# Kernel tuning notes

Hardware: AMD Instinct MI355X
Metric: run time of the kernel (lower is better)

## Reference

```python
import jax, jax.numpy as jnp
import numpy as np

DIM = 1024
N_HEADS = 16
N_KV = 4
HEAD_DIM = DIM // N_HEADS          # 64
GROUP = N_HEADS // N_KV            # 4
KV_DIM = N_KV * HEAD_DIM           # 256
B, S = 2, 2048


def setup_inputs() -> dict:
    key = jax.random.key(0)
    ks = jax.random.split(key, 5)
    scale = 1.0 / np.sqrt(DIM)
    return {
        "x": jax.random.normal(ks[0], (B, S, DIM), dtype=jnp.float32),
        "W_qkv": jax.random.normal(ks[1], (DIM, DIM + 2 * KV_DIM), dtype=jnp.float32) * scale,
        "b_qkv": jnp.zeros((DIM + 2 * KV_DIM,), dtype=jnp.float32),
        "W_out": jax.random.normal(ks[2], (DIM, DIM), dtype=jnp.float32) * scale,
        "b_out": jnp.zeros((DIM,), dtype=jnp.float32),
    }


def reference(x, W_qkv, b_qkv, W_out, b_out):
    b, s, d = x.shape
    qkv = x @ W_qkv + b_qkv                                   # [b, s, dim + 2*kv_dim]
    q, k, v = jnp.split(qkv, [DIM, DIM + KV_DIM], axis=-1)
    # q: [b, n_kv, group, s, hd]; k, v: [b, n_kv, s, hd]
    q = q.reshape(b, s, N_HEADS, HEAD_DIM).transpose(0, 2, 1, 3)
    q = q.reshape(b, N_KV, GROUP, s, HEAD_DIM)
    k = k.reshape(b, s, N_KV, HEAD_DIM).transpose(0, 2, 1, 3)
    v = v.reshape(b, s, N_KV, HEAD_DIM).transpose(0, 2, 1, 3)
    scores = jnp.einsum("bkgsd,bktd->bkgst", q, k) / np.sqrt(HEAD_DIM)
    causal = jnp.tril(jnp.ones((s, s), dtype=bool))           # [s, s]
    scores = jnp.where(causal, scores, -jnp.inf)
    attn = jax.nn.softmax(scores, axis=-1)                    # dropout = 0 (eval)
    y = jnp.einsum("bkgst,bktd->bkgsd", attn, v)              # [b, n_kv, g, s, hd]
    y = y.reshape(b, N_HEADS, s, HEAD_DIM).transpose(0, 2, 1, 3).reshape(b, s, d)
    return y @ W_out + b_out
```

## Files before the change

### kernel.cpp

```cpp
#include <hip/hip_runtime.h>
#include <cstdint>
#include <cstddef>

typedef __bf16 bf16x8 __attribute__((ext_vector_type(8)));
typedef __bf16 bf16x4 __attribute__((ext_vector_type(4)));
typedef float  f32x4  __attribute__((ext_vector_type(4)));

#define DIMD 1024
#define SEQ  2048
#define NB   2
#define NH   16
#define HD   64
#define QKVN 1536
#define VOFF 1280
#define VSTR 2080
#define CSC  0.18033688011112042f

typedef __attribute__((address_space(1))) const void* as1_cvp;
typedef __attribute__((address_space(3))) void* as3_vp;
#define GLL16(g, l) __builtin_amdgcn_global_load_lds((as1_cvp)(const void*)(g), (as3_vp)(void*)(l), 16, 0, 0)

__global__ __launch_bounds__(256) void prep(
    const float* __restrict__ x, __bf16* __restrict__ xb,
    const float* __restrict__ Wqkv, __bf16* __restrict__ wqkvT,
    const float* __restrict__ Wout, __bf16* __restrict__ woutT)
{
    __shared__ float t[32][33];
    const int bidx = blockIdx.x;
    const int tid  = threadIdx.x;

    if (bidx < 4096) {
        int i = bidx * 256 + tid;
        float4 v = reinterpret_cast<const float4*>(x)[i];
        bf16x4 o;
        o[0] = (__bf16)v.x; o[1] = (__bf16)v.y; o[2] = (__bf16)v.z; o[3] = (__bf16)v.w;
        reinterpret_cast<bf16x4*>(xb)[i] = o;
        return;
    }

    const float* in; __bf16* out; int C, bx, by;
    if (bidx < 5632) {
        int idx = bidx - 4096;
        in = Wqkv; out = wqkvT; C = QKVN;
        bx = idx % 48; by = idx / 48;
    } else {
        int idx = bidx - 5632;
        in = Wout; out = woutT; C = DIMD;
        bx = idx & 31; by = idx >> 5;
    }
    const int tx = tid & 31, ty = tid >> 5;
#pragma unroll
    for (int i = 0; i < 32; i += 8)
        t[ty + i][tx] = in[(size_t)(by * 32 + ty + i) * C + bx * 32 + tx];
    __syncthreads();
#pragma unroll
    for (int i = 0; i < 32; i += 8)
        out[(size_t)(bx * 32 + ty + i) * DIMD + by * 32 + tx] = (__bf16)t[tx][ty + i];
}

__global__ void transpose_v(const __bf16* __restrict__ qkv, __bf16* __restrict__ vtg) {
    __shared__ __bf16 t[32][34];
    const int z = blockIdx.z;
    const int b = z >> 2, kh = z & 3;
    const int s0 = blockIdx.x * 32, d0 = blockIdx.y * 32;
    const int tx = threadIdx.x, ty = threadIdx.y;
    const __bf16* src = qkv + (size_t)b * SEQ * QKVN + VOFF + kh * HD;
#pragma unroll
    for (int i = 0; i < 32; i += 8)
        t[ty + i][tx] = src[(size_t)(s0 + ty + i) * QKVN + d0 + tx];
    __syncthreads();
    __bf16* dst = vtg + ((size_t)z * HD + d0) * VSTR + s0;
#pragma unroll
    for (int i = 0; i < 32; i += 8)
        dst[(size_t)(ty + i) * VSTR + tx] = t[tx][ty + i];
}

template<int OUT_BF16, int QSCALE>
__global__ __launch_bounds__(256) void gemm_bf16(
    const __bf16* __restrict__ A, const __bf16* __restrict__ Bt,
    const float* __restrict__ bias, void* __restrict__ Cout,
    int M, int N, int K, int nx)
{
    __shared__ __bf16 Als[128 * 32];
    __shared__ __bf16 Bls[64 * 32];
    const int tid  = threadIdx.x;
    const int lane = tid & 63;
    const int wave = tid >> 6;
    const int lo = lane & 15, hi = lane >> 4;

    const int lin = blockIdx.x;
    const int cpx = gridDim.x >> 3;
    const int swz = (lin & 7) * cpx + (lin >> 3);
    const int bm = (swz / nx) * 128, bn = (swz % nx) * 64;
    const int wr = (wave >> 1) * 64, wc = (wave & 1) * 32;

    const __bf16* gA = A  + (size_t)(bm + wave * 16 + (lane >> 2)) * K + (lane & 3) * 8;
    const __bf16* gB = Bt + (size_t)(bn + wave * 16 + (lane >> 2)) * K + (lane & 3) * 8;
    __bf16* lA = &Als[wave * 16 * 32];
    __bf16* lB = &Bls[wave * 16 * 32];

    f32x4 acc[4][2] = {};

    for (int k0 = 0; k0 < K; k0 += 32) {
        __syncthreads();
        GLL16(gA + k0,                  lA);
        GLL16(gA + k0 + (size_t)64 * K, lA + 2048);
        GLL16(gB + k0,                  lB);
        __syncthreads();

        bf16x8 af[4], bfr[2];
#pragma unroll
        for (int i = 0; i < 4; i++)
            af[i] = *reinterpret_cast<const bf16x8*>(&Als[(wr + i * 16 + lo) * 32 + hi * 8]);
#pragma unroll
        for (int j = 0; j < 2; j++)
            bfr[j] = *reinterpret_cast<const bf16x8*>(&Bls[(wc + j * 16 + lo) * 32 + hi * 8]);
#pragma unroll
        for (int i = 0; i < 4; i++)
#pragma unroll
            for (int j = 0; j < 2; j++)
                acc[i][j] = __builtin_amdgcn_mfma_f32_16x16x32_bf16(af[i], bfr[j], acc[i][j], 0, 0, 0);
    }

#pragma unroll
    for (int j = 0; j < 2; j++) {
        int col = bn + wc + j * 16 + lo;
        float bv = bias[col];
#pragma unroll
        for (int i = 0; i < 4; i++) {
            int row0 = bm + wr + i * 16 + hi * 4;
#pragma unroll
            for (int rr = 0; rr < 4; rr++) {
                float v = acc[i][j][rr] + bv;
                if (QSCALE && col < DIMD) v *= CSC;
                if (OUT_BF16) ((__bf16*)Cout)[(size_t)(row0 + rr) * N + col] = (__bf16)v;
                else          ((float* )Cout)[(size_t)(row0 + rr) * N + col] = v;
            }
        }
    }
}

__global__ __launch_bounds__(512, 4) void attn_fwd(
    const __bf16* __restrict__ qkv, const __bf16* __restrict__ vt, __bf16* __restrict__ y)
{
    __shared__ __bf16 Kls[128 * 64];
    __shared__ __bf16 Vls[64 * 128];
    __shared__ __bf16 Pls[8][2][16][72];
    const int tid  = threadIdx.x;
    const int wave = tid >> 6, lane = tid & 63;
    const int lo = lane & 15, hi = lane >> 4;
    const int head = wave & 3, par = wave >> 2;

    const int bid = blockIdx.x;
    const int z  = bid & 7;
    const int b  = z >> 2, kh = z & 3;
    const int p  = bid >> 3;
    const int h  = kh * 4 + head;

    const int TA = p, TB = 127 - p;
    const int qwA = TA * 16, qwB = TB * 16;
    const int cA = (TA >> 2) + 1, cB = (TB >> 2) + 1;
    const int nsc = (cB + 1) >> 1;

    const __bf16* base = qkv + (size_t)b * SEQ * QKVN;
    const __bf16* qp = base + h * HD;
    const __bf16* kp = base + DIMD + kh * HD;
    const __bf16* vp = vt + (size_t)z * HD * VSTR;

    const int srow = lane >> 3;
    const int sun  = ((lane & 7) ^ srow) * 8;
    const __bf16* kst0 = kp + (size_t)(wave * 16 + srow) * QKVN + sun;
    const __bf16* kst1 = kp + (size_t)(wave * 16 + 8 + srow) * QKVN + sun;
    const int vrow = lane >> 4;
    const int vun0 = ((lane & 15) ^ vrow) * 8;
    const int vun1 = ((lane & 15) ^ (vrow + 4)) * 8;
    const __bf16* vst0 = vp + (size_t)(wave * 8 + vrow) * VSTR + vun0;
    const __bf16* vst1 = vp + (size_t)(wave * 8 + 4 + vrow) * VSTR + vun1;
    __bf16* kdst = &Kls[wave * 1024];
    __bf16* vdst = &Vls[wave * 1024];

#define STAGE(s)                                            \
    do {                                                    \
        const size_t ko = (size_t)(s) * 128 * QKVN;         \
        const int    vo = (s) * 128;                        \
        GLL16(kst0 + ko, kdst);                             \
        GLL16(kst1 + ko, kdst + 512);                       \
        GLL16(vst0 + vo, vdst);                             \
        GLL16(vst1 + vo, vdst + 512);                       \
    } while (0)

    const int xk = lo & 7;
    const int u0 = (hi ^ xk) * 8;
    const int u1 = ((hi + 4) ^ xk) * 8;
    const int kb = par * 64;

    bf16x8 bQA0 = *reinterpret_cast<const bf16x8*>(qp + (size_t)(qwA + lo) * QKVN + hi * 8);
    bf16x8 bQA1 = *reinterpret_cast<const bf16x8*>(qp + (size_t)(qwA + lo) * QKVN + 32 + hi * 8);
    bf16x8 bQB0 = *reinterpret_cast<const bf16x8*>(qp + (size_t)(qwB + lo) * QKVN + hi * 8);
    bf16x8 bQB1 = *reinterpret_cast<const bf16x8*>(qp + (size_t)(qwB + lo) * QKVN + 32 + hi * 8);

    f32x4 accA[4] = {}, accB[4] = {};
    float ssA = 0.0f, ssB = 0.0f;

    STAGE(0);
    __syncthreads();

    for (int s = 0; s < nsc; ++s) {
        const int ce = 2 * s + par;
        const int kt = ce << 6;
        const bool aB = (ce < cB), dB = (ce == cB - 1);
        const bool aA = (ce < cA), dA = (ce == cA - 1);

        if (aB) {
#pragma unroll
            for (int ks = 0; ks < 4; ks++) {
                const __bf16* Kr = &Kls[(kb + ks * 16 + lo) * 64];
                bf16x8 aK0 = *reinterpret_cast<const bf16x8*>(Kr + u0);
                bf16x8 aK1 = *reinterpret_cast<const bf16x8*>(Kr + u1);

                {
                    f32x4 sv = {0.f, 0.f, 0.f, 0.f};
                    sv = __builtin_amdgcn_mfma_f32_16x16x32_bf16(aK0, bQB0, sv, 0, 0, 0);
                    sv = __builtin_amdgcn_mfma_f32_16x16x32_bf16(aK1, bQB1, sv, 0, 0, 0);
                    bf16x4 pk;
#pragma unroll
                    for (int r = 0; r < 4; r++) {
                        float e = exp2f(sv[r]);
                        if (dB && (kt + ks * 16 + hi * 4 + r > qwB + lo)) e = 0.0f;
                        ssB += e;
                        pk[r] = (__bf16)e;
                    }
                    *reinterpret_cast<bf16x4*>(&Pls[wave][1][lo][ks * 16 + hi * 4]) = pk;
                }
                if (aA) {
                    f32x4 sv = {0.f, 0.f, 0.f, 0.f};
                    sv = __builtin_amdgcn_mfma_f32_16x16x32_bf16(aK0, bQA0, sv, 0, 0, 0);
                    sv = __builtin_amdgcn_mfma_f32_16x16x32_bf16(aK1, bQA1, sv, 0, 0, 0);
                    bf16x4 pk;
#pragma unroll
                    for (int r = 0; r < 4; r++) {
                        float e = exp2f(sv[r]);
                        if (dA && (kt + ks * 16 + hi * 4 + r > qwA + lo)) e = 0.0f;
                        ssA += e;
                        pk[r] = (__bf16)e;
                    }
                    *reinterpret_cast<bf16x4*>(&Pls[wave][0][lo][ks * 16 + hi * 4]) = pk;
                }
            }

#pragma unroll
            for (int k2 = 0; k2 < 2; k2++) {
                const int uv = ((8 * par + k2 * 4 + hi) ^ xk) * 8;
                bf16x8 v0 = *reinterpret_cast<const bf16x8*>(&Vls[(0 * 16 + lo) * 128] + uv);
                bf16x8 v1 = *reinterpret_cast<const bf16x8*>(&Vls[(1 * 16 + lo) * 128] + uv);
                bf16x8 v2 = *reinterpret_cast<const bf16x8*>(&Vls[(2 * 16 + lo) * 128] + uv);
                bf16x8 v3 = *reinterpret_cast<const bf16x8*>(&Vls[(3 * 16 + lo) * 128] + uv);
                bf16x8 pB = *reinterpret_cast<const bf16x8*>(&Pls[wave][1][lo][k2 * 32 + hi * 8]);
                accB[0] = __builtin_amdgcn_mfma_f32_16x16x32_bf16(pB, v0, accB[0], 0, 0, 0);
                accB[1] = __builtin_amdgcn_mfma_f32_16x16x32_bf16(pB, v1, accB[1], 0, 0, 0);
                accB[2] = __builtin_amdgcn_mfma_f32_16x16x32_bf16(pB, v2, accB[2], 0, 0, 0);
                accB[3] = __builtin_amdgcn_mfma_f32_16x16x32_bf16(pB, v3, accB[3], 0, 0, 0);
                if (aA) {
                    bf16x8 pA = *reinterpret_cast<const bf16x8*>(&Pls[wave][0][lo][k2 * 32 + hi * 8]);
                    accA[0] = __builtin_amdgcn_mfma_f32_16x16x32_bf16(pA, v0, accA[0], 0, 0, 0);
                    accA[1] = __builtin_amdgcn_mfma_f32_16x16x32_bf16(pA, v1, accA[1], 0, 0, 0);
                    accA[2] = __builtin_amdgcn_mfma_f32_16x16x32_bf16(pA, v2, accA[2], 0, 0, 0);
                    accA[3] = __builtin_amdgcn_mfma_f32_16x16x32_bf16(pA, v3, accA[3], 0, 0, 0);
                }
            }
        }

        __syncthreads();
        if (s + 1 < nsc) {
            STAGE(s + 1);
            __syncthreads();
        }
    }
#undef STAGE

    float* cls = (float*)&Pls[0][0][0][0];
    const int cbase = (head * 64 + lane) * 36;
    if (par == 1) {
#pragma unroll
        for (int f = 0; f < 4; f++) {
            *reinterpret_cast<f32x4*>(&cls[cbase + f * 4])      = accA[f];
            *reinterpret_cast<f32x4*>(&cls[cbase + 16 + f * 4]) = accB[f];
        }
        cls[cbase + 32] = ssA;
        cls[cbase + 33] = ssB;
    }
    __syncthreads();
    if (par == 0) {
#pragma unroll
        for (int f = 0; f < 4; f++) {
            accA[f] += *reinterpret_cast<f32x4*>(&cls[cbase + f * 4]);
            accB[f] += *reinterpret_cast<f32x4*>(&cls[cbase + 16 + f * 4]);
        }
        ssA += cls[cbase + 32];
        ssB += cls[cbase + 33];

        ssA += __shfl_xor(ssA, 16);  ssA += __shfl_xor(ssA, 32);
        ssB += __shfl_xor(ssB, 16);  ssB += __shfl_xor(ssB, 32);
#pragma unroll
        for (int r = 0; r < 4; r++) {
            float srA = __shfl(ssA, hi * 4 + r);
            float srB = __shfl(ssB, hi * 4 + r);
            float invA = 1.0f / srA, invB = 1.0f / srB;
            int qA = qwA + hi * 4 + r, qB = qwB + hi * 4 + r;
#pragma unroll
            for (int f = 0; f < 4; f++) {
                y[(size_t)(b * SEQ + qA) * DIMD + h * HD + f * 16 + lo] = (__bf16)(accA[f][r] * invA);
                y[(size_t)(b * SEQ + qB) * DIMD + h * HD + f * 16 + lo] = (__bf16)(accB[f][r] * invB);
            }
        }
    }
}

extern "C" void kernel_launch(void* const* d_in, const int* in_sizes, int n_in,
                              void* d_out, int out_size, void* d_ws, size_t ws_size,
                              hipStream_t stream) {
    const float* x    = (const float*)d_in[0];
    const float* Wqkv = (const float*)d_in[1];
    const float* bqkv = (const float*)d_in[2];
    const float* Wout = (const float*)d_in[3];
    const float* bout = (const float*)d_in[4];
    float* out = (float*)d_out;

    char* ws = (char*)d_ws;
    __bf16* xb    = (__bf16*)(ws);
    __bf16* wqkvT = (__bf16*)(ws + ((size_t)8  << 20));
    __bf16* woutT = (__bf16*)(ws + ((size_t)11 << 20));
    __bf16* qkvb  = (__bf16*)(ws + ((size_t)13 << 20));
    __bf16* vtg   = wqkvT;
    __bf16* yb    = xb;

    const int M = NB * SEQ;

    prep<<<6656, 256, 0, stream>>>(x, xb, Wqkv, wqkvT, Wout, woutT);

    gemm_bf16<1, 1><<<(M / 128) * (QKVN / 64), 256, 0, stream>>>(
        xb, wqkvT, bqkv, qkvb, M, QKVN, DIMD, QKVN / 64);

    transpose_v<<<dim3(SEQ / 32, HD / 32, NB * 4), dim3(32, 8), 0, stream>>>(qkvb, vtg);

    attn_fwd<<<512, 512, 0, stream>>>(qkvb, vtg, yb);

    gemm_bf16<0, 0><<<(M / 128) * (DIMD / 64), 256, 0, stream>>>(
        yb, woutT, bout, out, M, DIMD, DIMD, DIMD / 64);
}
```

Before: 104.0 us.

## Double-buffer K/V tiles and keep P in registers via transposed PV MFMA

Doubles the K/V shared-memory buffers so the next tile's async global-to-LDS loads are issued before computing on the current tile, removing one barrier per iteration. The P-through-LDS round trip is dropped by computing O^T with 16x16x16 MFMAs that take the exp'd scores directly from registers as the B operand, with V as the A operand. Output stores become vectorized bf16x4 writes along the transposed layout. This trades wider MFMAs for more, smaller ones, raises LDS use, and needs a correct swizzled V fragment indexing.

```diff
diff --git a/kernel.cpp b/kernel.cpp
--- a/kernel.cpp
+++ b/kernel.cpp
@@ -5,6 +5,7 @@
 typedef __bf16 bf16x8 __attribute__((ext_vector_type(8)));
 typedef __bf16 bf16x4 __attribute__((ext_vector_type(4)));
 typedef float  f32x4  __attribute__((ext_vector_type(4)));
+typedef short  s16x4  __attribute__((ext_vector_type(4)));
 
 #define DIMD 1024
 #define SEQ  2048
@@ -143,9 +144,8 @@
 __global__ __launch_bounds__(512, 4) void attn_fwd(
     const __bf16* __restrict__ qkv, const __bf16* __restrict__ vt, __bf16* __restrict__ y)
 {
-    __shared__ __bf16 Kls[128 * 64];
-    __shared__ __bf16 Vls[64 * 128];
-    __shared__ __bf16 Pls[8][2][16][72];
+    __shared__ __bf16 Ka[2][8192];
+    __shared__ __bf16 Va[2][8192];
     const int tid  = threadIdx.x;
     const int wave = tid >> 6, lane = tid & 63;
     const int lo = lane & 15, hi = lane >> 4;
@@ -176,23 +176,26 @@
     const int vun1 = ((lane & 15) ^ (vrow + 4)) * 8;
     const __bf16* vst0 = vp + (size_t)(wave * 8 + vrow) * VSTR + vun0;
     const __bf16* vst1 = vp + (size_t)(wave * 8 + 4 + vrow) * VSTR + vun1;
-    __bf16* kdst = &Kls[wave * 1024];
-    __bf16* vdst = &Vls[wave * 1024];
-
-#define STAGE(s)                                            \
-    do {                                                    \
-        const size_t ko = (size_t)(s) * 128 * QKVN;         \
-        const int    vo = (s) * 128;                        \
-        GLL16(kst0 + ko, kdst);                             \
-        GLL16(kst1 + ko, kdst + 512);                       \
-        GLL16(vst0 + vo, vdst);                             \
-        GLL16(vst1 + vo, vdst + 512);                       \
+    __bf16* kdst = &Ka[0][wave * 1024];
+    __bf16* vdst = &Va[0][wave * 1024];
+
+#define STAGE(s, buf)                                              \
+    do {                                                           \
+        const size_t ko = (size_t)(s) * 128 * QKVN;                \
+        const int    vo = (s) * 128;                               \
+        GLL16(kst0 + ko, kdst + (buf) * 8192);                     \
+        GLL16(kst1 + ko, kdst + (buf) * 8192 + 512);               \
+        GLL16(vst0 + vo, vdst + (buf) * 8192);                     \
+        GLL16(vst1 + vo, vdst + (buf) * 8192 + 512);               \
     } while (0)
 
     const int xk = lo & 7;
     const int u0 = (hi ^ xk) * 8;
     const int u1 = ((hi + 4) ^ xk) * 8;
-    const int kb = par * 64;
+    int voff[4];
+#pragma unroll
+    for (int ks = 0; ks < 4; ks++)
+        voff[ks] = (((par * 8 + ks * 2 + (hi >> 1)) ^ xk) << 3) + (hi & 1) * 4;
 
     bf16x8 bQA0 = *reinterpret_cast<const bf16x8*>(qp + (size_t)(qwA + lo) * QKVN + hi * 8);
     bf16x8 bQA1 = *reinterpret_cast<const bf16x8*>(qp + (size_t)(qwA + lo) * QKVN + 32 + hi * 8);
@@ -200,85 +203,79 @@
     bf16x8 bQB1 = *reinterpret_cast<const bf16x8*>(qp + (size_t)(qwB + lo) * QKVN + 32 + hi * 8);
 
     f32x4 accA[4] = {}, accB[4] = {};
-    float ssA = 0.0f, ssB = 0.0f;
-
-    STAGE(0);
+    f32x4 ssvA = {0.f, 0.f, 0.f, 0.f}, ssvB = {0.f, 0.f, 0.f, 0.f};
+
+    STAGE(0, 0);
     __syncthreads();
 
+    int cur = 0;
     for (int s = 0; s < nsc; ++s) {
+        if (s + 1 < nsc) STAGE(s + 1, cur ^ 1);
+
         const int ce = 2 * s + par;
         const int kt = ce << 6;
         const bool aB = (ce < cB), dB = (ce == cB - 1);
         const bool aA = (ce < cA), dA = (ce == cA - 1);
 
         if (aB) {
+            const __bf16* Kb = &Ka[cur][par * 4096];
+            const __bf16* Vb = &Va[cur][0];
+
 #pragma unroll
             for (int ks = 0; ks < 4; ks++) {
-                const __bf16* Kr = &Kls[(kb + ks * 16 + lo) * 64];
+                const __bf16* Kr = Kb + (ks * 16 + lo) * 64;
                 bf16x8 aK0 = *reinterpret_cast<const bf16x8*>(Kr + u0);
                 bf16x8 aK1 = *reinterpret_cast<const bf16x8*>(Kr + u1);
 
-                {
-                    f32x4 sv = {0.f, 0.f, 0.f, 0.f};
-                    sv = __builtin_amdgcn_mfma_f32_16x16x32_bf16(aK0, bQB0, sv, 0, 0, 0);
-                    sv = __builtin_amdgcn_mfma_f32_16x16x32_bf16(aK1, bQB1, sv, 0, 0, 0);
-                    bf16x4 pk;
-#pragma unroll
-                    for (int r = 0; r < 4; r++) {
-                        float e = exp2f(sv[r]);
-                        if (dB && (kt + ks * 16 + hi * 4 + r > qwB + lo)) e = 0.0f;
-                        ssB += e;
-                        pk[r] = (__bf16)e;
-                    }
-                    *reinterpret_cast<bf16x4*>(&Pls[wave][1][lo][ks * 16 + hi * 4]) = pk;
+                f32x4 svB = {0.f, 0.f, 0.f, 0.f};
+                svB = __builtin_amdgcn_mfma_f32_16x16x32_bf16(aK0, bQB0, svB, 0, 0, 0);
+                svB = __builtin_amdgcn_mfma_f32_16x16x32_bf16(aK1, bQB1, svB, 0, 0, 0);
+                f32x4 svA = {0.f, 0.f, 0.f, 0.f};
+                if (aA) {
+                    svA = __builtin_amdgcn_mfma_f32_16x16x32_bf16(aK0, bQA0, svA, 0, 0, 0);
+                    svA = __builtin_amdgcn_mfma_f32_16x16x32_bf16(aK1, bQA1, svA, 0, 0, 0);
+                }
+
+                bf16x4 pkB, pkA;
+#pragma unroll
+                for (int r = 0; r < 4; r++) {
+                    float eB = exp2f(svB[r]);
+                    if (dB && (kt + ks * 16 + hi * 4 + r > qwB + lo)) eB = 0.0f;
+                    ssvB[r] += eB;
+                    pkB[r] = (__bf16)eB;
                 }
                 if (aA) {
-                    f32x4 sv = {0.f, 0.f, 0.f, 0.f};
-                    sv = __builtin_amdgcn_mfma_f32_16x16x32_bf16(aK0, bQA0, sv, 0, 0, 0);
-                    sv = __builtin_amdgcn_mfma_f32_16x16x32_bf16(aK1, bQA1, sv, 0, 0, 0);
-                    bf16x4 pk;
 #pragma unroll
                     for (int r = 0; r < 4; r++) {
-                        float e = exp2f(sv[r]);
-                        if (dA && (kt + ks * 16 + hi * 4 + r > qwA + lo)) e = 0.0f;
-                        ssA += e;
-                        pk[r] = (__bf16)e;
+                        float eA = exp2f(svA[r]);
+                        if (dA && (kt + ks * 16 + hi * 4 + r > qwA + lo)) eA = 0.0f;
+                        ssvA[r] += eA;
+                        pkA[r] = (__bf16)eA;
                     }
-                    *reinterpret_cast<bf16x4*>(&Pls[wave][0][lo][ks * 16 + hi * 4]) = pk;
+                }
+
+#pragma unroll
+                for (int f = 0; f < 4; f++) {
+                    bf16x4 vf = *reinterpret_cast<const bf16x4*>(&Vb[(f * 16 + lo) * 128] + voff[ks]);
+                    s16x4 vfi = __builtin_bit_cast(s16x4, vf);
+                    accB[f] = __builtin_amdgcn_mfma_f32_16x16x16bf16_1k(
+                        vfi, __builtin_bit_cast(s16x4, pkB), accB[f], 0, 0, 0);
+                    if (aA)
+                        accA[f] = __builtin_amdgcn_mfma_f32_16x16x16bf16_1k(
+                            vfi, __builtin_bit_cast(s16x4, pkA), accA[f], 0, 0, 0);
                 }
             }
-
-#pragma unroll
-            for (int k2 = 0; k2 < 2; k2++) {
-                const int uv = ((8 * par + k2 * 4 + hi) ^ xk) * 8;
-                bf16x8 v0 = *reinterpret_cast<const bf16x8*>(&Vls[(0 * 16 + lo) * 128] + uv);
-                bf16x8 v1 = *reinterpret_cast<const bf16x8*>(&Vls[(1 * 16 + lo) * 128] + uv);
-                bf16x8 v2 = *reinterpret_cast<const bf16x8*>(&Vls[(2 * 16 + lo) * 128] + uv);
-                bf16x8 v3 = *reinterpret_cast<const bf16x8*>(&Vls[(3 * 16 + lo) * 128] + uv);
-                bf16x8 pB = *reinterpret_cast<const bf16x8*>(&Pls[wave][1][lo][k2 * 32 + hi * 8]);
-                accB[0] = __builtin_amdgcn_mfma_f32_16x16x32_bf16(pB, v0, accB[0], 0, 0, 0);
-                accB[1] = __builtin_amdgcn_mfma_f32_16x16x32_bf16(pB, v1, accB[1], 0, 0, 0);
-                accB[2] = __builtin_amdgcn_mfma_f32_16x16x32_bf16(pB, v2, accB[2], 0, 0, 0);
-                accB[3] = __builtin_amdgcn_mfma_f32_16x16x32_bf16(pB, v3, accB[3], 0, 0, 0);
-                if (aA) {
-                    bf16x8 pA = *reinterpret_cast<const bf16x8*>(&Pls[wave][0][lo][k2 * 32 + hi * 8]);
-                    accA[0] = __builtin_amdgcn_mfma_f32_16x16x32_bf16(pA, v0, accA[0], 0, 0, 0);
-                    accA[1] = __builtin_amdgcn_mfma_f32_16x16x32_bf16(pA, v1, accA[1], 0, 0, 0);
-                    accA[2] = __builtin_amdgcn_mfma_f32_16x16x32_bf16(pA, v2, accA[2], 0, 0, 0);
-                    accA[3] = __builtin_amdgcn_mfma_f32_16x16x32_bf16(pA, v3, accA[3], 0, 0, 0);
-                }
-            }
         }
 
         __syncthreads();
-        if (s + 1 < nsc) {
-            STAGE(s + 1);
-            __syncthreads();
-        }
+        cur ^= 1;
     }
 #undef STAGE
 
-    float* cls = (float*)&Pls[0][0][0][0];
+    float ssA = (ssvA[0] + ssvA[1]) + (ssvA[2] + ssvA[3]);
+    float ssB = (ssvB[0] + ssvB[1]) + (ssvB[2] + ssvB[3]);
+
+    float* cls = (float*)&Ka[0][0];
     const int cbase = (head * 64 + lane) * 36;
     if (par == 1) {
 #pragma unroll
@@ -293,25 +290,27 @@
     if (par == 0) {
 #pragma unroll
         for (int f = 0; f < 4; f++) {
-            accA[f] += *reinterpret_cast<f32x4*>(&cls[cbase + f * 4]);
-            accB[f] += *reinterpret_cast<f32x4*>(&cls[cbase + 16 + f * 4]);
+            accA[f] += *reinterpret_cast<const f32x4*>(&cls[cbase + f * 4]);
+            accB[f] += *reinterpret_cast<const f32x4*>(&cls[cbase + 16 + f * 4]);
         }
         ssA += cls[cbase + 32];
         ssB += cls[cbase + 33];
 
         ssA += __shfl_xor(ssA, 16);  ssA += __shfl_xor(ssA, 32);
         ssB += __shfl_xor(ssB, 16);  ssB += __shfl_xor(ssB, 32);
-#pragma unroll
-        for (int r = 0; r < 4; r++) {
-            float srA = __shfl(ssA, hi * 4 + r);
-            float srB = __shfl(ssB, hi * 4 + r);
-            float invA = 1.0f / srA, invB = 1.0f / srB;
-            int qA = qwA + hi * 4 + r, qB = qwB + hi * 4 + r;
-#pragma unroll
-            for (int f = 0; f < 4; f++) {
-                y[(size_t)(b * SEQ + qA) * DIMD + h * HD + f * 16 + lo] = (__bf16)(accA[f][r] * invA);
-                y[(size_t)(b * SEQ + qB) * DIMD + h * HD + f * 16 + lo] = (__bf16)(accB[f][r] * invB);
+        float invA = 1.0f / ssA, invB = 1.0f / ssB;
+        const size_t ybA = (size_t)(b * SEQ + qwA + lo) * DIMD + h * HD + hi * 4;
+        const size_t ybB = (size_t)(b * SEQ + qwB + lo) * DIMD + h * HD + hi * 4;
+#pragma unroll
+        for (int f = 0; f < 4; f++) {
+            bf16x4 oa, ob;
+#pragma unroll
+            for (int r = 0; r < 4; r++) {
+                oa[r] = (__bf16)(accA[f][r] * invA);
+                ob[r] = (__bf16)(accB[f][r] * invB);
             }
+            *reinterpret_cast<bf16x4*>(&y[ybA + f * 16]) = oa;
+            *reinterpret_cast<bf16x4*>(&y[ybB + f * 16]) = ob;
         }
     }
 }
```

Result: slower. 254.0 us (+144.2%).
